# Kernel optimization log

Hardware: AMD Instinct MI355X
Metric: run time of the kernel (lower is better)

Reference implementation:

```python
import jax, jax.numpy as jnp
import numpy as np

DIM = 512
EPS = 1e-8
LN_EPS = 1e-5


def _layernorm(x, g, b):
    mu = jnp.mean(x, axis=-1, keepdims=True)
    var = jnp.mean(jnp.square(x - mu), axis=-1, keepdims=True)
    return (x - mu) * jax.lax.rsqrt(var + LN_EPS) * g + b


def setup_inputs() -> dict:
    key = jax.random.key(0)
    ks = jax.random.split(key, 8)
    b, i, j, d = 8, 2048, 2048, DIM
    s = 1.0 / np.sqrt(d)
    return {
        "inputs": jax.random.normal(ks[0], (b, i, d), dtype=jnp.float32),
        "context": jax.random.normal(ks[1], (b, j, d), dtype=jnp.float32),
        "g_in": jnp.ones((d,), jnp.float32),
        "b_in": jnp.zeros((d,), jnp.float32),
        "g_ctx": jnp.ones((d,), jnp.float32),
        "b_ctx": jnp.zeros((d,), jnp.float32),
        "Wq": jax.random.uniform(ks[2], (d, d), jnp.float32, -s, s),
        "bq": jnp.zeros((d,), jnp.float32),
        "Wk": jax.random.uniform(ks[3], (d, d), jnp.float32, -s, s),
        "bk": jnp.zeros((d,), jnp.float32),
        "Wv": jax.random.uniform(ks[4], (d, d), jnp.float32, -s, s),
        "bv": jnp.zeros((d,), jnp.float32),
    }


def reference(inputs, context, g_in, b_in, g_ctx, b_ctx, Wq, bq, Wk, bk, Wv, bv):
    scale = DIM ** (-0.5)
    x = _layernorm(inputs, g_in, b_in)
    c = _layernorm(context, g_ctx, b_ctx)
    q = x @ Wq + bq          # [b,i,d]
    k = c @ Wk + bk          # [b,j,d]
    v = c @ Wv + bv          # [b,j,d]
    dots = jnp.einsum('bid,bjd->bij', q, k) * scale
    # NOTE: non-standard softmax over the QUERY axis (dim=1), then eps shift
    attn = jax.nn.softmax(dots, axis=1) + EPS
    # second renormalization over the KEY axis (dim=2)
    mean_attn = attn / (jnp.sum(attn, axis=2, keepdims=True) + EPS)
    updates = jnp.einsum('bjd,bij->bid', v, mean_attn)
    return updates
```

## Files before the change

### kernel.cpp

```cpp
#include <hip/hip_runtime.h>
#include <hip/hip_bf16.h>
#include <math.h>

#define EPSF 1e-8f
#define LN_EPSF 1e-5f
#define SCALE_QK 0.04419417382415922f

typedef unsigned short ushort_t;
typedef __bf16 bhalf;
typedef bhalf bhalf8 __attribute__((ext_vector_type(8)));
typedef float f32x4 __attribute__((ext_vector_type(4)));

__device__ __forceinline__ float b2f(ushort_t u) {
    return __uint_as_float((unsigned)u << 16);
}
__device__ __forceinline__ ushort_t f2b(float f) {
    unsigned x = __float_as_uint(f);
    return (ushort_t)((x + 0x7fffu + ((x >> 16) & 1u)) >> 16);
}
__device__ __forceinline__ unsigned pk2(float lo, float hi) {
    return (unsigned)f2b(lo) | ((unsigned)f2b(hi) << 16);
}
__device__ __forceinline__ void gload16(const ushort_t* g, ushort_t* l) {
    __builtin_amdgcn_global_load_lds(
        (const __attribute__((address_space(1))) unsigned int*)g,
        (__attribute__((address_space(3))) unsigned int*)l, 16, 0, 0);
}

#define WAITV(N) { asm volatile("s_waitcnt vmcnt(" #N ")" ::: "memory"); \
                   __builtin_amdgcn_sched_barrier(0); }
#define FENCE_LGKM { asm volatile("s_waitcnt lgkmcnt(0)" ::: "memory"); \
                     __builtin_amdgcn_sched_barrier(0); }

__global__ __launch_bounds__(256) void mv_bias_kernel(
    const float* __restrict__ Wq, const float* __restrict__ Wk,
    const float* __restrict__ bq, const float* __restrict__ bk,
    float* __restrict__ wqbk, float* __restrict__ wkbq, float* __restrict__ cc)
{
    __shared__ float ls[4];
    const int y = blockIdx.y;
    const int t = threadIdx.x;
    if (y == 2) {
        if (blockIdx.x != 0) return;
        float s = bq[t] * bk[t] + bq[t + 256] * bk[t + 256];
#pragma unroll
        for (int off = 32; off > 0; off >>= 1) s += __shfl_down(s, off, 64);
        int lane = t & 63, w = t >> 6;
        if (lane == 0) ls[w] = s;
        __syncthreads();
        if (t == 0) cc[0] = ls[0] + ls[1] + ls[2] + ls[3];
        return;
    }
    const float* W = y ? Wk : Wq;
    const float* v = y ? bq : bk;
    float* o = y ? wkbq : wqbk;
    const int row = blockIdx.x * 16 + (t >> 4);
    const int l = t & 15;
    const float* wr = W + (size_t)row * 512 + l * 32;
    const float* vr = v + l * 32;
    float s = 0.f;
#pragma unroll
    for (int c = 0; c < 32; ++c) s += wr[c] * vr[c];
#pragma unroll
    for (int off = 8; off > 0; off >>= 1) s += __shfl_down(s, off, 16);
    if (l == 0) o[row] = s;
}

__global__ __launch_bounds__(256) void ln_apply_kernel(
    const float* __restrict__ X1, const float* __restrict__ X2,
    const float* __restrict__ g1, const float* __restrict__ b1,
    const float* __restrict__ g2, const float* __restrict__ b2,
    const float* __restrict__ wb1, const float* __restrict__ wb2,
    ushort_t* __restrict__ O1, ushort_t* __restrict__ O2,
    float* __restrict__ T1, float* __restrict__ T2)
{
    const bool sec = blockIdx.y != 0;
    const float* X = sec ? X2 : X1;
    const float* g = sec ? g2 : g1;
    const float* b = sec ? b2 : b1;
    const float* wb = sec ? wb2 : wb1;
    ushort_t* O = sec ? O2 : O1;
    float* T = sec ? T2 : T1;
    const size_t base = (size_t)blockIdx.x * 512;
    const int t = threadIdx.x;
    float2 x = ((const float2*)(X + base))[t];
    float s = x.x + x.y;
    float q = fmaf(x.x, x.x, x.y * x.y);
#pragma unroll
    for (int off = 32; off > 0; off >>= 1) {
        s += __shfl_down(s, off, 64);
        q += __shfl_down(q, off, 64);
    }
    __shared__ float ls[4], lq[4], mv[2], ld[4];
    int lane = t & 63, w = t >> 6;
    if (lane == 0) { ls[w] = s; lq[w] = q; }
    __syncthreads();
    if (t == 0) {
        float st = ls[0] + ls[1] + ls[2] + ls[3];
        float qt = lq[0] + lq[1] + lq[2] + lq[3];
        float mu = st * (1.0f / 512.0f);
        float var = qt * (1.0f / 512.0f) - mu * mu;
        mv[0] = mu;
        mv[1] = rsqrtf(var + LN_EPSF);
    }
    __syncthreads();
    const float mu = mv[0], rstd = mv[1];
    float2 gg = ((const float2*)g)[t];
    float2 bb = ((const float2*)b)[t];
    float2 ww = ((const float2*)wb)[t];
    float o0 = (x.x - mu) * rstd * gg.x + bb.x;
    float o1 = (x.y - mu) * rstd * gg.y + bb.y;
    ((unsigned*)O)[blockIdx.x * 256 + t] = pk2(o0, o1);
    float d = o0 * ww.x + o1 * ww.y;
#pragma unroll
    for (int off = 32; off > 0; off >>= 1) d += __shfl_down(d, off, 64);
    if (lane == 0) ld[w] = d;
    __syncthreads();
    if (t == 0) T[blockIdx.x] = ld[0] + ld[1] + ld[2] + ld[3];
}

__global__ __launch_bounds__(256) void wprep_kernel(
    const float* __restrict__ Wq, const float* __restrict__ Wk,
    const float* __restrict__ Wv,
    ushort_t* __restrict__ Wqb, ushort_t* __restrict__ Wkb,
    ushort_t* __restrict__ WvT)
{
    const int z = blockIdx.z;
    if (z < 2) {
        const float* W = z ? Wk : Wq;
        ushort_t* T = z ? Wkb : Wqb;
        size_t idx = ((size_t)(blockIdx.y * 16 + blockIdx.x)) * 1024 + threadIdx.x * 4;
        float4 f = *(const float4*)(W + idx);
        uint2 u;
        u.x = pk2(f.x, f.y);
        u.y = pk2(f.z, f.w);
        *(uint2*)(T + idx) = u;
        return;
    }
    __shared__ float tile[32][33];
    int tx = threadIdx.x & 31, ty = threadIdx.x >> 5;
    int r0 = blockIdx.y * 32, c0 = blockIdx.x * 32;
#pragma unroll
    for (int p = 0; p < 4; ++p)
        tile[ty + p * 8][tx] = Wv[(size_t)(r0 + ty + p * 8) * 512 + c0 + tx];
    __syncthreads();
#pragma unroll
    for (int p = 0; p < 4; ++p)
        WvT[(size_t)(c0 + ty + p * 8) * 512 + r0 + tx] = f2b(tile[tx][ty + p * 8]);
}

__global__ __launch_bounds__(256) void colrecip_kernel(
    const float* __restrict__ cs, float* __restrict__ cr,
    ushort_t* __restrict__ crs)
{
    int t = blockIdx.x * 256 + threadIdx.x;
    float r = 1.0f / cs[t];
    cr[t] = r;
    crs[t] = f2b(r);
}

__global__ __launch_bounds__(512) void gemm256_exp_kernel(
    const ushort_t* __restrict__ A, const ushort_t* __restrict__ B,
    ushort_t* __restrict__ Cout,
    const float* __restrict__ t1, const float* __restrict__ t2,
    const float* __restrict__ cc, float* __restrict__ colsum,
    int K, int N, size_t strideA, size_t strideB, size_t strideC,
    float scale)
{
    __shared__ __align__(16) ushort_t As0[256 * 64];
    __shared__ __align__(16) ushort_t As1[256 * 64];
    __shared__ __align__(16) ushort_t Bs0[256 * 64];
    __shared__ __align__(16) ushort_t Bs1[256 * 64];
    const int tid = threadIdx.x;

    const int nbx = gridDim.x, nby = gridDim.y;
    const int nwg = nbx * nby * gridDim.z;
    int lin = blockIdx.x + nbx * (blockIdx.y + nby * blockIdx.z);
    int swz = (lin & 7) * (nwg >> 3) + (lin >> 3);
    const int sx = __builtin_ctz(nbx), sy = __builtin_ctz(nby);
    const int bx = swz & (nbx - 1);
    const int by = (swz >> sx) & (nby - 1);
    const int bz = swz >> (sx + sy);

    const ushort_t* Ab = A + strideA * bz;
    const ushort_t* Bb = B + strideB * bz;
    const int m0 = by * 256;
    const int n0 = bx * 256;
    const int wave = tid >> 6;
    const int lane = tid & 63;
    const int fm = lane & 15;
    const int fq = lane >> 4;
    const int fq4 = fq * 4;
    const int wm = (wave >> 2) * 128;
    const int wn = (wave & 3) * 64;

    const int lrow = lane >> 3;
    const int lchunk = lane & 7;
    const int scs = lchunk ^ lrow;

    const ushort_t* aSrc[4]; const ushort_t* bSrc[4];
#pragma unroll
    for (int p = 0; p < 4; ++p) {
        int row = wave * 32 + p * 8 + lrow;
        aSrc[p] = Ab + (size_t)(m0 + row) * K + scs * 8;
        bSrc[p] = Bb + (size_t)(n0 + row) * K + scs * 8;
    }
    const int dOff = wave * 2048 + lane * 8;

    const int cBase = fq ^ (fm & 7);

    f32x4 acc[8][4];
#pragma unroll
    for (int i = 0; i < 8; ++i)
#pragma unroll
        for (int j = 0; j < 4; ++j) acc[i][j] = (f32x4){0.f, 0.f, 0.f, 0.f};

    auto stage = [&](ushort_t* Ad, ushort_t* Bd, int k0) {
#pragma unroll
        for (int p = 0; p < 4; ++p) {
            gload16(aSrc[p] + k0, Ad + dOff + p * 512);
            gload16(bSrc[p] + k0, Bd + dOff + p * 512);
        }
    };
    auto compute = [&](const ushort_t* Asb, const ushort_t* Bsb) {
#pragma unroll
        for (int s = 0; s < 2; ++s) {
            const int off = ((cBase ^ (s << 2)) << 3);
            bhalf8 af[8], bfr[4];
#pragma unroll
            for (int u = 0; u < 8; ++u)
                af[u] = *(const bhalf8*)(Asb + (wm + u * 16 + fm) * 64 + off);
#pragma unroll
            for (int u = 0; u < 4; ++u)
                bfr[u] = *(const bhalf8*)(Bsb + (wn + u * 16 + fm) * 64 + off);
#pragma unroll
            for (int i = 0; i < 8; ++i)
#pragma unroll
                for (int j = 0; j < 4; ++j)
                    acc[i][j] = __builtin_amdgcn_mfma_f32_16x16x32_bf16(
                        bfr[j], af[i], acc[i][j], 0, 0, 0);
        }
    };

    const int nk = K >> 6;
    stage(As0, Bs0, 0);
    stage(As1, Bs1, 64);
    for (int t = 0; t < nk - 2; t += 2) {
        WAITV(8);
        __builtin_amdgcn_s_barrier();
        compute(As0, Bs0);
        FENCE_LGKM;
        __builtin_amdgcn_s_barrier();
        stage(As0, Bs0, (t + 2) << 6);
        WAITV(8);
        __builtin_amdgcn_s_barrier();
        compute(As1, Bs1);
        FENCE_LGKM;
        __builtin_amdgcn_s_barrier();
        stage(As1, Bs1, (t + 3) << 6);
    }
    WAITV(8);
    __builtin_amdgcn_s_barrier();
    compute(As0, Bs0);
    WAITV(0);
    __builtin_amdgcn_s_barrier();
    compute(As1, Bs1);

    ushort_t* C = Cout + strideC * bz;
    const float cv = cc[0];
    f32x4 t2c[4];
#pragma unroll
    for (int nj = 0; nj < 4; ++nj) {
        float4 tv = *(const float4*)(t2 + (size_t)bz * 2048 +
                                     n0 + wn + nj * 16 + fq4);
        t2c[nj][0] = tv.x + cv;
        t2c[nj][1] = tv.y + cv;
        t2c[nj][2] = tv.z + cv;
        t2c[nj][3] = tv.w + cv;
    }
    float psum[4][4];
#pragma unroll
    for (int nj = 0; nj < 4; ++nj)
#pragma unroll
        for (int r = 0; r < 4; ++r) psum[nj][r] = 0.f;
#pragma unroll
    for (int mi = 0; mi < 8; ++mi) {
        const int row = m0 + wm + mi * 16 + fm;
        const float t1v = t1[(size_t)bz * 2048 + row];
        ushort_t* Cr = C + (size_t)row * N + n0 + wn + fq4;
#pragma unroll
        for (int nj = 0; nj < 4; ++nj) {
            ushort_t h0 = f2b(__expf((acc[mi][nj][0] + t1v + t2c[nj][0]) * scale));
            ushort_t h1 = f2b(__expf((acc[mi][nj][1] + t1v + t2c[nj][1]) * scale));
            ushort_t h2 = f2b(__expf((acc[mi][nj][2] + t1v + t2c[nj][2]) * scale));
            ushort_t h3 = f2b(__expf((acc[mi][nj][3] + t1v + t2c[nj][3]) * scale));
            uint2 u;
            u.x = (unsigned)h0 | ((unsigned)h1 << 16);
            u.y = (unsigned)h2 | ((unsigned)h3 << 16);
            *(uint2*)(Cr + nj * 16) = u;
            psum[nj][0] += b2f(h0);
            psum[nj][1] += b2f(h1);
            psum[nj][2] += b2f(h2);
            psum[nj][3] += b2f(h3);
        }
    }
#pragma unroll
    for (int nj = 0; nj < 4; ++nj)
#pragma unroll
        for (int r = 0; r < 4; ++r) {
            float v = psum[nj][r];
            v += __shfl_xor(v, 1, 64);
            v += __shfl_xor(v, 2, 64);
            v += __shfl_xor(v, 4, 64);
            v += __shfl_xor(v, 8, 64);
            psum[nj][r] = v;
        }
    float* colpart = (float*)&As0[0];
    __syncthreads();
    if (tid < 256) colpart[tid] = 0.f;
    __syncthreads();
    if (fm == 0) {
#pragma unroll
        for (int nj = 0; nj < 4; ++nj)
#pragma unroll
            for (int r = 0; r < 4; ++r)
                atomicAdd(&colpart[wn + nj * 16 + fq4 + r], psum[nj][r]);
    }
    __syncthreads();
    if (tid < 256)
        atomicAdd(&colsum[(size_t)bz * 2048 + n0 + tid], colpart[tid]);
}

__global__ __launch_bounds__(512) void gemm_out256_kernel(
    const ushort_t* __restrict__ A, const ushort_t* __restrict__ B,
    float* __restrict__ Cout, const ushort_t* __restrict__ crs,
    int K, int N, size_t strideA, size_t strideB, size_t strideC)
{
    __shared__ __align__(16) ushort_t As0[256 * 64];
    __shared__ __align__(16) ushort_t As1[256 * 64];
    __shared__ __align__(16) ushort_t Bs0[128 * 64];
    __shared__ __align__(16) ushort_t Bs1[128 * 64];
    __shared__ __align__(16) ushort_t crs_lds[2048];
    const int tid = threadIdx.x;

    const int nbx = gridDim.x, nby = gridDim.y;
    const int nwg = nbx * nby * gridDim.z;
    int lin = blockIdx.x + nbx * (blockIdx.y + nby * blockIdx.z);
    int swz = (lin & 7) * (nwg >> 3) + (lin >> 3);
    const int sx = __builtin_ctz(nbx), sy = __builtin_ctz(nby);
    const int bx = swz & (nbx - 1);
    const int by = (swz >> sx) & (nby - 1);
    const int bz = swz >> (sx + sy);

    const ushort_t* Ab = A + strideA * bz;
    const ushort_t* Bb = B + strideB * bz;
    const int m0 = by * 256;
    const int n0 = bx * 128;
    const int wave = tid >> 6;
    const int lane = tid & 63;
    const int fm = lane & 15;
    const int fq = lane >> 4;
    const int fq4 = fq * 4;
    const int wm = (wave >> 1) * 64;
    const int wn = (wave & 1) * 64;

    const int lrow = lane >> 3;
    const int lchunk = lane & 7;
    const int scs = lchunk ^ lrow;

    const ushort_t* aSrc[4]; const ushort_t* bSrc[2];
#pragma unroll
    for (int p = 0; p < 4; ++p) {
        int row = wave * 32 + p * 8 + lrow;
        aSrc[p] = Ab + (size_t)(m0 + row) * K + scs * 8;
    }
#pragma unroll
    for (int p = 0; p < 2; ++p) {
        int row = wave * 16 + p * 8 + lrow;
        bSrc[p] = Bb + (size_t)(n0 + row) * K + scs * 8;
    }
    const int aOff = wave * 2048 + lane * 8;
    const int bOff = wave * 1024 + lane * 8;

    if (tid < 256) {
        uint4 c4 = *(const uint4*)(crs + (size_t)bz * 2048 + tid * 8);
        *(uint4*)&crs_lds[tid * 8] = c4;
    }
    __syncthreads();

    const int cBase = fq ^ (fm & 7);

    f32x4 acc[4][4];
    f32x4 sacc[4];
#pragma unroll
    for (int i = 0; i < 4; ++i) {
        sacc[i] = (f32x4){0.f, 0.f, 0.f, 0.f};
#pragma unroll
        for (int j = 0; j < 4; ++j) acc[i][j] = (f32x4){0.f, 0.f, 0.f, 0.f};
    }

    auto stage = [&](ushort_t* Ad, ushort_t* Bd, int k0) {
#pragma unroll
        for (int p = 0; p < 4; ++p)
            gload16(aSrc[p] + k0, Ad + aOff + p * 512);
#pragma unroll
        for (int p = 0; p < 2; ++p)
            gload16(bSrc[p] + k0, Bd + bOff + p * 512);
    };
    auto compute = [&](const ushort_t* Asb, const ushort_t* Bsb, int k0) {
#pragma unroll
        for (int s = 0; s < 2; ++s) {
            const int off = ((cBase ^ (s << 2)) << 3);
            bhalf8 af[4], bfr[4];
#pragma unroll
            for (int u = 0; u < 4; ++u) {
                af[u]  = *(const bhalf8*)(Asb + (wm + u * 16 + fm) * 64 + off);
                bfr[u] = *(const bhalf8*)(Bsb + (wn + u * 16 + fm) * 64 + off);
            }
#pragma unroll
            for (int i = 0; i < 4; ++i)
#pragma unroll
                for (int j = 0; j < 4; ++j)
                    acc[i][j] = __builtin_amdgcn_mfma_f32_16x16x32_bf16(
                        bfr[j], af[i], acc[i][j], 0, 0, 0);
            bhalf8 bc = *(const bhalf8*)&crs_lds[k0 + (s << 5) + (fq << 3)];
#pragma unroll
            for (int i = 0; i < 4; ++i)
                sacc[i] = __builtin_amdgcn_mfma_f32_16x16x32_bf16(
                    bc, af[i], sacc[i], 0, 0, 0);
        }
    };

    const int nk = K >> 6;
    stage(As0, Bs0, 0);
    stage(As1, Bs1, 64);
    for (int t = 0; t < nk - 2; t += 2) {
        WAITV(6);
        __builtin_amdgcn_s_barrier();
        compute(As0, Bs0, t << 6);
        FENCE_LGKM;
        __builtin_amdgcn_s_barrier();
        stage(As0, Bs0, (t + 2) << 6);
        WAITV(6);
        __builtin_amdgcn_s_barrier();
        compute(As1, Bs1, (t + 1) << 6);
        FENCE_LGKM;
        __builtin_amdgcn_s_barrier();
        stage(As1, Bs1, (t + 3) << 6);
    }
    WAITV(6);
    __builtin_amdgcn_s_barrier();
    compute(As0, Bs0, (nk - 2) << 6);
    WAITV(0);
    __builtin_amdgcn_s_barrier();
    compute(As1, Bs1, (nk - 1) << 6);

    float* C = Cout + strideC * bz;
#pragma unroll
    for (int ti = 0; ti < 4; ++ti) {
        const int row = m0 + wm + ti * 16 + fm;
        const float rs = 1.0f / (sacc[ti][0] + 2.049e-5f);
        float* Cr = C + (size_t)row * N + n0 + wn + fq4;
#pragma unroll
        for (int tj = 0; tj < 4; ++tj) {
            f32x4 v;
#pragma unroll
            for (int r = 0; r < 4; ++r) v[r] = acc[ti][tj][r] * rs;
            *(f32x4*)(Cr + tj * 16) = v;
        }
    }
}

template <int MODE>
__global__ __launch_bounds__(256) void mfma_gemm_kernel(
    const ushort_t* __restrict__ A, const ushort_t* __restrict__ B,
    void* __restrict__ Cout,
    const float* __restrict__ bias,
    const float* __restrict__ crcol,
    int K, int N, size_t strideA, size_t strideB, size_t strideC)
{
    __shared__ __align__(16) ushort_t As[128 * 64];
    __shared__ __align__(16) ushort_t Bs[128 * 64];
    const int tid = threadIdx.x;

    const int nbx = gridDim.x, nby = gridDim.y, nbz = gridDim.z;
    const int nwg = nbx * nby * nbz;
    int bx, by, bz;
    if ((nwg & 7) == 0) {
        int lin = blockIdx.x + nbx * (blockIdx.y + nby * blockIdx.z);
        int swz = (lin & 7) * (nwg >> 3) + (lin >> 3);
        const int sx = __builtin_ctz(nbx), sy = __builtin_ctz(nby);
        bx = swz & (nbx - 1);
        by = (swz >> sx) & (nby - 1);
        bz = swz >> (sx + sy);
    } else {
        bx = blockIdx.x; by = blockIdx.y; bz = blockIdx.z;
    }

    const ushort_t* Ab = A + strideA * bz;
    const ushort_t* Bb = B + strideB * bz;
    const int m0 = by * 128;
    const int n0 = bx * 128;
    const int wave = tid >> 6;
    const int lane = tid & 63;
    const int fm = lane & 15;
    const int fq = lane >> 4;
    const int fq4 = fq * 4;
    const int fm7 = fm & 7;
    const int wm = (wave >> 1) * 64;
    const int wn = (wave & 1) * 64;

    const int lrow = lane >> 3;
    const int lchunk = lane & 7;
    const int scs = lchunk ^ lrow;

    const ushort_t* aSrc[4]; const ushort_t* bSrc[4];
    ushort_t* aDst[4]; ushort_t* bDst[4];
#pragma unroll
    for (int p = 0; p < 4; ++p) {
        int row = wave * 32 + p * 8 + lrow;
        aSrc[p] = Ab + (size_t)(m0 + row) * K + scs * 8;
        bSrc[p] = Bb + (size_t)(n0 + row) * K + scs * 8;
        aDst[p] = As + (wave * 32 + p * 8) * 64 + lane * 8;
        bDst[p] = Bs + (wave * 32 + p * 8) * 64 + lane * 8;
    }

    const int cBase = fq ^ fm7;
    const ushort_t* aFrag[4]; const ushort_t* bFrag[4];
#pragma unroll
    for (int t = 0; t < 4; ++t) {
        aFrag[t] = As + (wm + t * 16 + fm) * 64;
        bFrag[t] = Bs + (wn + t * 16 + fm) * 64;
    }

    f32x4 acc[4][4];
#pragma unroll
    for (int i = 0; i < 4; ++i)
#pragma unroll
        for (int j = 0; j < 4; ++j) acc[i][j] = (f32x4){0.f, 0.f, 0.f, 0.f};

    for (int k0 = 0; k0 < K; k0 += 64) {
        __syncthreads();
#pragma unroll
        for (int p = 0; p < 4; ++p) {
            gload16(aSrc[p] + k0, aDst[p]);
            gload16(bSrc[p] + k0, bDst[p]);
        }
        __syncthreads();
#pragma unroll
        for (int s = 0; s < 2; ++s) {
            const int off = ((cBase ^ (s << 2)) << 3);
            bhalf8 af[4], bfr[4];
#pragma unroll
            for (int u = 0; u < 4; ++u) {
                af[u]  = *(const bhalf8*)(aFrag[u] + off);
                bfr[u] = *(const bhalf8*)(bFrag[u] + off);
            }
#pragma unroll
            for (int i = 0; i < 4; ++i)
#pragma unroll
                for (int j = 0; j < 4; ++j)
                    acc[i][j] = __builtin_amdgcn_mfma_f32_16x16x32_bf16(
                        bfr[j], af[i], acc[i][j], 0, 0, 0);
        }
    }

    if (MODE == 3) {
        ushort_t* C = (ushort_t*)Cout + strideC * bz;
        f32x4 crv[4];
#pragma unroll
        for (int tj = 0; tj < 4; ++tj) {
            float4 cq = *(const float4*)(crcol + (size_t)bz * 2048 +
                                         n0 + wn + tj * 16 + fq4);
            crv[tj][0] = cq.x; crv[tj][1] = cq.y;
            crv[tj][2] = cq.z; crv[tj][3] = cq.w;
        }
#pragma unroll
        for (int ti = 0; ti < 4; ++ti) {
            const int row = m0 + wm + ti * 16 + fm;
            const float bvv = bias[row];
            ushort_t* Cr = C + (size_t)row * N + n0 + wn + fq4;
#pragma unroll
            for (int tj = 0; tj < 4; ++tj) {
                uint2 u;
                u.x = pk2((acc[ti][tj][0] + bvv) * crv[tj][0],
                          (acc[ti][tj][1] + bvv) * crv[tj][1]);
                u.y = pk2((acc[ti][tj][2] + bvv) * crv[tj][2],
                          (acc[ti][tj][3] + bvv) * crv[tj][3]);
                *(uint2*)(Cr + tj * 16) = u;
            }
        }
    } else {
        ushort_t* C = (ushort_t*)Cout + strideC * bz;
#pragma unroll
        for (int ti = 0; ti < 4; ++ti) {
            const int row = m0 + wm + ti * 16 + fm;
            ushort_t* Cr = C + (size_t)row * N + n0 + wn + fq4;
#pragma unroll
            for (int tj = 0; tj < 4; ++tj) {
                uint2 u;
                u.x = pk2(acc[ti][tj][0], acc[ti][tj][1]);
                u.y = pk2(acc[ti][tj][2], acc[ti][tj][3]);
                *(uint2*)(Cr + tj * 16) = u;
            }
        }
    }
}

extern "C" void kernel_launch(void* const* d_in, const int* in_sizes, int n_in,
                              void* d_out, int out_size, void* d_ws, size_t ws_size,
                              hipStream_t stream)
{
    const float* inputs  = (const float*)d_in[0];
    const float* context = (const float*)d_in[1];
    const float* g_in    = (const float*)d_in[2];
    const float* b_in    = (const float*)d_in[3];
    const float* g_ctx   = (const float*)d_in[4];
    const float* b_ctx   = (const float*)d_in[5];
    const float* Wq      = (const float*)d_in[6];
    const float* bq      = (const float*)d_in[7];
    const float* Wk      = (const float*)d_in[8];
    const float* bk      = (const float*)d_in[9];
    const float* Wv      = (const float*)d_in[10];
    const float* bv      = (const float*)d_in[11];
    float* out = (float*)d_out;

    const size_t QKV  = 8ull * 2048 * 512;
    const size_t WSZ  = 512ull * 512;
    const size_t DOTS = 8ull * 2048 * 2048;

    ushort_t* xln   = (ushort_t*)d_ws;
    ushort_t* cln   = xln + QKV;
    ushort_t* Wqb   = cln + QKV;
    ushort_t* Wkb   = Wqb + WSZ;
    ushort_t* WvT   = Wkb + WSZ;
    ushort_t* Mb    = WvT + WSZ;
    ushort_t* KM    = Mb + WSZ;
    ushort_t* vTs   = KM + QKV;
    ushort_t* edots = vTs + QKV;
    ushort_t* crs   = edots + DOTS;
    float* fbase    = (float*)(crs + 16384);
    float* colsum   = fbase;
    float* colrecip = colsum + 16384;
    float* t1       = colrecip + 16384;
    float* t2       = t1 + 16384;
    float* wqbk     = t2 + 16384;
    float* wkbq     = wqbk + 512;
    float* cc       = wkbq + 512;
    size_t need_bytes = (4 * QKV + 4 * WSZ + DOTS + 16384) * 2
                      + (4 * 16384 + 1024 + 1) * 4;
    if (ws_size < need_bytes) return;

    hipMemsetAsync(colsum, 0, 16384 * sizeof(float), stream);

    mv_bias_kernel<<<dim3(32, 3), 256, 0, stream>>>(Wq, Wk, bq, bk, wqbk, wkbq, cc);

    ln_apply_kernel<<<dim3(16384, 2), 256, 0, stream>>>(
        inputs, context, g_in, b_in, g_ctx, b_ctx, wqbk, wkbq, xln, cln, t1, t2);

    wprep_kernel<<<dim3(16, 16, 3), 256, 0, stream>>>(Wq, Wk, Wv, Wqb, Wkb, WvT);

    mfma_gemm_kernel<0><<<dim3(4, 4, 1), 256, 0, stream>>>(
        Wqb, Wkb, Mb, nullptr, nullptr,
        512, 512, 0, 0, 0);

    mfma_gemm_kernel<0><<<dim3(4, 128, 1), 256, 0, stream>>>(
        cln, Mb, KM, nullptr, nullptr,
        512, 512, 0, 0, 0);

    gemm256_exp_kernel<<<dim3(8, 8, 8), 512, 0, stream>>>(
        xln, KM, edots, t1, t2, cc, colsum,
        512, 2048, (size_t)2048 * 512, (size_t)2048 * 512, (size_t)2048 * 2048,
        SCALE_QK);

    colrecip_kernel<<<64, 256, 0, stream>>>(colsum, colrecip, crs);

    mfma_gemm_kernel<3><<<dim3(16, 4, 8), 256, 0, stream>>>(
        WvT, cln, vTs, bv, colrecip,
        512, 2048, 0, (size_t)2048 * 512, (size_t)512 * 2048);

    gemm_out256_kernel<<<dim3(4, 8, 8), 512, 0, stream>>>(
        edots, vTs, out, crs,
        2048, 512, (size_t)2048 * 2048, (size_t)512 * 2048, (size_t)2048 * 512);
}
```

Before: 298.8 us.

## Interleave global-to-LDS staging with quarter-tile MFMA phases in GEMM main loop

Restructures the 256x256 bf16 GEMM main loop so that each K-step is split into four quadrant MFMA phases. Slices of the next tile's A/B global-to-LDS loads are issued between those phases, and s_setprio raises wave priority during MFMA bursts. This replaces the coarse stage-then-compute double buffering and is meant to keep the matrix units busy while memory loads are in flight. It adds more barriers and complex vmcnt accounting, which risks stalls or races if the wait counts are wrong.

```diff
diff --git a/kernel.cpp b/kernel.cpp
--- a/kernel.cpp
+++ b/kernel.cpp
@@ -198,14 +198,10 @@
     const int lchunk = lane & 7;
     const int scs = lchunk ^ lrow;
 
-    const ushort_t* aSrc[4]; const ushort_t* bSrc[4];
-#pragma unroll
-    for (int p = 0; p < 4; ++p) {
-        int row = wave * 32 + p * 8 + lrow;
-        aSrc[p] = Ab + (size_t)(m0 + row) * K + scs * 8;
-        bSrc[p] = Bb + (size_t)(n0 + row) * K + scs * 8;
-    }
-    const int dOff = wave * 2048 + lane * 8;
+    const int aI  = (wave < 4) ? 2 * wave : 2 * wave + 8;
+    const int aII = (wave < 4) ? 8 + 2 * wave : 16 + 2 * wave;
+    const int bI  = (wave >> 1) * 8 + (wave & 1) * 2;
+    const int bII = bI + 4;
 
     const int cBase = fq ^ (fm & 7);
 
@@ -215,56 +211,132 @@
 #pragma unroll
         for (int j = 0; j < 4; ++j) acc[i][j] = (f32x4){0.f, 0.f, 0.f, 0.f};
 
-    auto stage = [&](ushort_t* Ad, ushort_t* Bd, int k0) {
-#pragma unroll
-        for (int p = 0; p < 4; ++p) {
-            gload16(aSrc[p] + k0, Ad + dOff + p * 512);
-            gload16(bSrc[p] + k0, Bd + dOff + p * 512);
-        }
+    auto rdA = [&](const ushort_t* R, int u, int s) {
+        return *(const bhalf8*)(R + (wm + u * 16 + fm) * 64 +
+                                ((cBase ^ (s << 2)) << 3));
     };
-    auto compute = [&](const ushort_t* Asb, const ushort_t* Bsb) {
-#pragma unroll
-        for (int s = 0; s < 2; ++s) {
-            const int off = ((cBase ^ (s << 2)) << 3);
-            bhalf8 af[8], bfr[4];
-#pragma unroll
-            for (int u = 0; u < 8; ++u)
-                af[u] = *(const bhalf8*)(Asb + (wm + u * 16 + fm) * 64 + off);
-#pragma unroll
-            for (int u = 0; u < 4; ++u)
-                bfr[u] = *(const bhalf8*)(Bsb + (wn + u * 16 + fm) * 64 + off);
-#pragma unroll
-            for (int i = 0; i < 8; ++i)
-#pragma unroll
-                for (int j = 0; j < 4; ++j)
-                    acc[i][j] = __builtin_amdgcn_mfma_f32_16x16x32_bf16(
-                        bfr[j], af[i], acc[i][j], 0, 0, 0);
-        }
+    auto rdB = [&](const ushort_t* R, int u, int s) {
+        return *(const bhalf8*)(R + (wn + u * 16 + fm) * 64 +
+                                ((cBase ^ (s << 2)) << 3));
     };
+    auto stA = [&](ushort_t* W, int s, int k0) {
+        gload16(Ab + (size_t)(m0 + s * 8 + lrow) * K + scs * 8 + k0,
+                W + s * 512 + lane * 8);
+    };
+    auto stB = [&](ushort_t* W, int s, int k0) {
+        gload16(Bb + (size_t)(n0 + s * 8 + lrow) * K + scs * 8 + k0,
+                W + s * 512 + lane * 8);
+    };
+
+    bhalf8 af[8], b0[4], b1[4];
+
+#define MFMA_Q(IH, JH, BF)                                                   \
+    _Pragma("unroll") for (int s = 0; s < 2; ++s)                            \
+    _Pragma("unroll") for (int i = 0; i < 4; ++i)                            \
+    _Pragma("unroll") for (int j = 0; j < 2; ++j)                            \
+        acc[(IH) * 4 + i][(JH) * 2 + j] =                                    \
+            __builtin_amdgcn_mfma_f32_16x16x32_bf16(                         \
+                BF[j * 2 + s], af[i * 2 + s], acc[(IH) * 4 + i][(JH) * 2 + j],\
+                0, 0, 0);
+
+#define TILE_MAIN(RA, RB, WA, WB, K0N)                                       \
+  {                            \
+    _Pragma("unroll") for (int u = 0; u < 4; ++u)                            \
+    _Pragma("unroll") for (int s = 0; s < 2; ++s) af[u * 2 + s] = rdA(RA, u, s); \
+    _Pragma("unroll") for (int u = 0; u < 2; ++u)                            \
+    _Pragma("unroll") for (int s = 0; s < 2; ++s) b0[u * 2 + s] = rdB(RB, u, s); \
+    stA(WA, aI, K0N); stA(WA, aI + 1, K0N);                                  \
+    WAITV(4);                                                                \
+    __builtin_amdgcn_s_barrier();                                            \
+    FENCE_LGKM;                                                              \
+    __builtin_amdgcn_s_setprio(1);                                           \
+    MFMA_Q(0, 0, b0);                                                        \
+    __builtin_amdgcn_s_setprio(0);                                           \
+    __builtin_amdgcn_s_barrier();                                            \
+                                   \
+    _Pragma("unroll") for (int u = 0; u < 2; ++u)                            \
+    _Pragma("unroll") for (int s = 0; s < 2; ++s) b1[u * 2 + s] = rdB(RB, u + 2, s); \
+    stB(WB, bI, K0N); stB(WB, bI + 1, K0N);                                  \
+    WAITV(4);                                                                \
+    __builtin_amdgcn_s_barrier();                                            \
+    FENCE_LGKM;                                                              \
+    __builtin_amdgcn_s_setprio(1);                                           \
+    MFMA_Q(0, 1, b1);                                                        \
+    __builtin_amdgcn_s_setprio(0);                                           \
+    __builtin_amdgcn_s_barrier();                                            \
+                                 \
+    _Pragma("unroll") for (int u = 0; u < 4; ++u)                            \
+    _Pragma("unroll") for (int s = 0; s < 2; ++s) af[u * 2 + s] = rdA(RA, u + 4, s); \
+    stB(WB, bII, K0N); stB(WB, bII + 1, K0N);                                \
+    __builtin_amdgcn_s_barrier();                                            \
+    FENCE_LGKM;                                                              \
+    __builtin_amdgcn_s_setprio(1);                                           \
+    MFMA_Q(1, 1, b1);                                                        \
+    __builtin_amdgcn_s_setprio(0);                                           \
+    __builtin_amdgcn_s_barrier();                                            \
+                                            \
+    stA(WA, aII, K0N); stA(WA, aII + 1, K0N);                                \
+    WAITV(4);                                                                \
+    __builtin_amdgcn_s_barrier();                                            \
+    __builtin_amdgcn_s_setprio(1);                                           \
+    MFMA_Q(1, 0, b0);                                                        \
+    __builtin_amdgcn_s_setprio(0);                                           \
+    __builtin_amdgcn_s_barrier();                                            \
+  }
+
+#define TILE_LAST(RA, RB)                                                    \
+  { _Pragma("unroll") for (int u = 0; u < 4; ++u)                            \
+    _Pragma("unroll") for (int s = 0; s < 2; ++s) af[u * 2 + s] = rdA(RA, u, s); \
+    _Pragma("unroll") for (int u = 0; u < 2; ++u)                            \
+    _Pragma("unroll") for (int s = 0; s < 2; ++s) b0[u * 2 + s] = rdB(RB, u, s); \
+    WAITV(2);                                                                \
+    __builtin_amdgcn_s_barrier();                                            \
+    FENCE_LGKM;                                                              \
+    __builtin_amdgcn_s_setprio(1);                                           \
+    MFMA_Q(0, 0, b0);                                                        \
+    __builtin_amdgcn_s_setprio(0);                                           \
+    __builtin_amdgcn_s_barrier();                                            \
+    _Pragma("unroll") for (int u = 0; u < 2; ++u)                            \
+    _Pragma("unroll") for (int s = 0; s < 2; ++s) b1[u * 2 + s] = rdB(RB, u + 2, s); \
+    WAITV(0);                                                                \
+    __builtin_amdgcn_s_barrier();                                            \
+    FENCE_LGKM;                                                              \
+    __builtin_amdgcn_s_setprio(1);                                           \
+    MFMA_Q(0, 1, b1);                                                        \
+    __builtin_amdgcn_s_setprio(0);                                           \
+    __builtin_amdgcn_s_barrier();                                            \
+    _Pragma("unroll") for (int u = 0; u < 4; ++u)                            \
+    _Pragma("unroll") for (int s = 0; s < 2; ++s) af[u * 2 + s] = rdA(RA, u + 4, s); \
+    __builtin_amdgcn_s_barrier();                                            \
+    FENCE_LGKM;                                                              \
+    __builtin_amdgcn_s_setprio(1);                                           \
+    MFMA_Q(1, 1, b1);                                                        \
+    __builtin_amdgcn_s_setprio(0);                                           \
+    __builtin_amdgcn_s_barrier();                                            \
+    __builtin_amdgcn_s_setprio(1);                                           \
+    MFMA_Q(1, 0, b0);                                                        \
+    __builtin_amdgcn_s_setprio(0);                                           \
+    __builtin_amdgcn_s_barrier();                                            \
+  }
 
     const int nk = K >> 6;
-    stage(As0, Bs0, 0);
-    stage(As1, Bs1, 64);
+    stA(As0, aI, 0); stA(As0, aI + 1, 0);
+    stB(Bs0, bI, 0); stB(Bs0, bI + 1, 0);
+    stB(Bs0, bII, 0); stB(Bs0, bII + 1, 0);
+    stA(As0, aII, 0); stA(As0, aII + 1, 0);
+    WAITV(4);
+    __builtin_amdgcn_s_barrier();
+
     for (int t = 0; t < nk - 2; t += 2) {
-        WAITV(8);
-        __builtin_amdgcn_s_barrier();
-        compute(As0, Bs0);
-        FENCE_LGKM;
-        __builtin_amdgcn_s_barrier();
-        stage(As0, Bs0, (t + 2) << 6);
-        WAITV(8);
-        __builtin_amdgcn_s_barrier();
-        compute(As1, Bs1);
-        FENCE_LGKM;
-        __builtin_amdgcn_s_barrier();
-        stage(As1, Bs1, (t + 3) << 6);
-    }
-    WAITV(8);
-    __builtin_amdgcn_s_barrier();
-    compute(As0, Bs0);
-    WAITV(0);
-    __builtin_amdgcn_s_barrier();
-    compute(As1, Bs1);
+        TILE_MAIN(As0, Bs0, As1, Bs1, (t + 1) << 6);
+        TILE_MAIN(As1, Bs1, As0, Bs0, (t + 2) << 6);
+    }
+    TILE_MAIN(As0, Bs0, As1, Bs1, (nk - 1) << 6);
+    TILE_LAST(As1, Bs1);
+
+#undef TILE_MAIN
+#undef TILE_LAST
+#undef MFMA_Q
 
     ushort_t* C = Cout + strideC * bz;
     const float cv = cc[0];
```

Result: slower. 307.2 us (+2.8%).
